# Kernel optimization log

Hardware: AMD Instinct MI355X
Metric: run time of the kernel (lower is better)

Reference implementation:

```python
import math
import jax, jax.numpy as jnp
import numpy as np

DIM = 1024
HEADS = 16
HEAD_DIM = DIM // HEADS
NEG = -10000.0


def setup_inputs() -> dict:
    key = jax.random.key(0)
    ks = jax.random.split(key, 9)
    B, S = 2, 2048
    s = 1.0 / math.sqrt(DIM)
    inp = {
        "x": jax.random.normal(ks[0], (B, S, DIM), dtype=jnp.float32),
        "Wq": jax.random.normal(ks[1], (DIM, DIM), dtype=jnp.float32) * s,
        "bq": jnp.zeros((DIM,), dtype=jnp.float32),
        "Wk": jax.random.normal(ks[2], (DIM, DIM), dtype=jnp.float32) * s,
        "bk": jnp.zeros((DIM,), dtype=jnp.float32),
        "Wv": jax.random.normal(ks[3], (DIM, DIM), dtype=jnp.float32) * s,
        "bv": jnp.zeros((DIM,), dtype=jnp.float32),
        "Wo": jax.random.normal(ks[4], (DIM, DIM), dtype=jnp.float32) * s,
        "bo": jnp.zeros((DIM,), dtype=jnp.float32),
    }
    return inp


def reference(x, Wq, bq, Wk, bk, Wv, bv, Wo, bo):
    B, S, D = x.shape
    q = x @ Wq + bq
    k = x @ Wk + bk
    v = x @ Wv + bv
    # [B, H, S, hd]
    def split_heads(t):
        return t.reshape(B, S, HEADS, HEAD_DIM).transpose(0, 2, 1, 3)
    q, k, v = split_heads(q), split_heads(k), split_heads(v)
    scores = jnp.einsum("bhqd,bhkd->bhqk", q, k) / math.sqrt(HEAD_DIM)
    causal = jnp.tril(jnp.ones((S, S), dtype=bool))  # [S, S]
    scores = jnp.where(causal[None, None], scores, NEG)
    probs = jax.nn.softmax(scores, axis=-1)
    ctx = jnp.einsum("bhqk,bhkd->bhqd", probs, v)  # [B, H, S, hd]
    ctx = ctx.transpose(0, 2, 1, 3).reshape(B, S, D)
    out = ctx @ Wo + bo
    return out
```

## Files before the change

### kernel.cpp

```cpp
#include <hip/hip_runtime.h>
#include <hip/hip_bf16.h>
#include <math.h>

#define DIMX 1024
#define HEADSX 16
#define HDX 64
#define BBX 2
#define SSX 2048
#define MMX (BBX*SSX)

typedef __bf16 bf16x8 __attribute__((ext_vector_type(8)));
typedef __bf16 bf16x4 __attribute__((ext_vector_type(4)));
typedef float  f32x4  __attribute__((ext_vector_type(4)));

#define NEGF (-1e30f)
#define QSCALE 0.18033688011112042f

static __device__ __forceinline__ void gload16(const void* g, void* l) {
  __builtin_amdgcn_global_load_lds(
      (const __attribute__((address_space(1))) unsigned int*)g,
      (__attribute__((address_space(3))) unsigned int*)l, 16, 0, 0);
}

__global__ __launch_bounds__(256) void k_convert_x(const float* __restrict__ x,
                                                   __bf16* __restrict__ xb) {
  int i = (blockIdx.x * 256 + threadIdx.x) * 4;
  float4 v = *(const float4*)&x[i];
  bf16x4 o = { (__bf16)v.x, (__bf16)v.y, (__bf16)v.z, (__bf16)v.w };
  *(bf16x4*)&xb[i] = o;
}

__global__ __launch_bounds__(256) void k_transpose_w(
    const float* __restrict__ Wq, const float* __restrict__ Wk,
    const float* __restrict__ Wv, const float* __restrict__ Wo,
    __bf16* __restrict__ wqkvT, __bf16* __restrict__ woT) {
  __shared__ __bf16 tile[64][65];
  const int mat = blockIdx.y;
  const float* src = (mat == 0) ? Wq : (mat == 1) ? Wk : (mat == 2) ? Wv : Wo;
  __bf16* dst = (mat < 3) ? (wqkvT + (size_t)mat * DIMX * DIMX) : woT;
  const int tx = blockIdx.x & 15, ty = blockIdx.x >> 4;
  const int k0 = ty * 64, n0 = tx * 64;
  #pragma unroll
  for (int rep = 0; rep < 16; ++rep) {
    int idx = rep * 256 + threadIdx.x;
    int r = idx >> 6, c = idx & 63;
    tile[r][c] = (__bf16)src[(size_t)(k0 + r) * DIMX + n0 + c];
  }
  __syncthreads();
  #pragma unroll
  for (int rep = 0; rep < 16; ++rep) {
    int idx = rep * 256 + threadIdx.x;
    int r = idx >> 6, c = idx & 63;
    dst[(size_t)(n0 + r) * DIMX + k0 + c] = tile[c][r];
  }
}

__global__ __launch_bounds__(256) void k_gemm_qkv(
    const __bf16* __restrict__ A,
    const __bf16* __restrict__ Bt,
    const float* __restrict__ b0, const float* __restrict__ b1,
    const float* __restrict__ b2,
    __bf16* __restrict__ qb, __bf16* __restrict__ kb, __bf16* __restrict__ vtb) {
  constexpr int BK = 32, K = 1024;
  __shared__ __bf16 As[128 * BK];
  __shared__ __bf16 Bs[128 * BK];
  const int tid = threadIdx.x, lane = tid & 63, wave = tid >> 6;
  const int g = lane >> 4, r16 = lane & 15;
  const int wm = wave & 1, wn = wave >> 1;
  const int id = blockIdx.x;
  const int xcd = id & 7, j96 = id >> 3;
  const int m0 = (xcd * 4 + (j96 & 3)) * 128;
  const int n0 = (j96 >> 2) * 128;

  f32x4 acc[4][4] = {};

  for (int k0 = 0; k0 < K; k0 += BK) {
    __syncthreads();
    #pragma unroll
    for (int i = 0; i < 2; ++i) {
      int c = wave * 64 + lane + 256 * i;
      gload16(&A [(size_t)(m0 + (c >> 2)) * K + k0 + (c & 3) * 8],
              (char*)As + (size_t)(wave * 64 + 256 * i) * 16);
      gload16(&Bt[(size_t)(n0 + (c >> 2)) * K + k0 + (c & 3) * 8],
              (char*)Bs + (size_t)(wave * 64 + 256 * i) * 16);
    }
    __syncthreads();
    bf16x8 af[4], bfr[4];
    #pragma unroll
    for (int i = 0; i < 4; ++i)
      af[i]  = *(const bf16x8*)&As[(wm * 64 + i * 16 + r16) * BK + g * 8];
    #pragma unroll
    for (int j = 0; j < 4; ++j)
      bfr[j] = *(const bf16x8*)&Bs[(wn * 64 + j * 16 + r16) * BK + g * 8];
    #pragma unroll
    for (int i = 0; i < 4; ++i)
      #pragma unroll
      for (int j = 0; j < 4; ++j)
        acc[i][j] = __builtin_amdgcn_mfma_f32_16x16x32_bf16(af[i], bfr[j],
                                                            acc[i][j], 0, 0, 0);
  }

  #pragma unroll
  for (int i = 0; i < 4; ++i) {
    #pragma unroll
    for (int j = 0; j < 4; ++j) {
      #pragma unroll
      for (int r = 0; r < 4; ++r) {
        int m = m0 + wm * 64 + i * 16 + 4 * g + r;
        int n = n0 + wn * 64 + j * 16 + r16;
        float v = acc[i][j][r];
        int proj = n >> 10, w = n & 1023, h = w >> 6, d = w & 63;
        const float* bp = (proj == 0) ? b0 : (proj == 1) ? b1 : b2;
        v += bp[w];
        int b = m >> 11, s = m & 2047, bh = b * HEADSX + h;
        if (proj == 0)      qb [((size_t)bh * SSX + s) * HDX + d] =
                                (__bf16)(v * QSCALE);
        else if (proj == 1) kb [((size_t)bh * SSX + s) * HDX + d] = (__bf16)v;
        else                vtb[((size_t)bh * HDX + d) * SSX + s] = (__bf16)v;
      }
    }
  }
}

__global__ __launch_bounds__(256) void k_gemm_out(
    const __bf16* __restrict__ A,
    const __bf16* __restrict__ Bt,
    const float* __restrict__ bias, float* __restrict__ outf) {
  constexpr int BK = 32, K = 1024;
  __shared__ __bf16 As[64 * BK];
  __shared__ __bf16 Bs[64 * BK];
  const int tid = threadIdx.x, lane = tid & 63, wave = tid >> 6;
  const int g = lane >> 4, r16 = lane & 15;
  const int wm = wave & 1, wn = wave >> 1;
  const int id = blockIdx.x;
  const int xcd = id & 7, j128 = id >> 3;
  const int m0 = (xcd * 8 + (j128 & 7)) * 64;
  const int n0 = (j128 >> 3) * 64;

  f32x4 acc[2][2] = {};

  for (int k0 = 0; k0 < K; k0 += BK) {
    __syncthreads();
    {
      int c = tid;
      gload16(&A [(size_t)(m0 + (c >> 2)) * K + k0 + (c & 3) * 8],
              (char*)As + (size_t)(wave * 64) * 16);
      gload16(&Bt[(size_t)(n0 + (c >> 2)) * K + k0 + (c & 3) * 8],
              (char*)Bs + (size_t)(wave * 64) * 16);
    }
    __syncthreads();
    bf16x8 af[2], bfr[2];
    #pragma unroll
    for (int i = 0; i < 2; ++i)
      af[i]  = *(const bf16x8*)&As[(wm * 32 + i * 16 + r16) * BK + g * 8];
    #pragma unroll
    for (int j = 0; j < 2; ++j)
      bfr[j] = *(const bf16x8*)&Bs[(wn * 32 + j * 16 + r16) * BK + g * 8];
    #pragma unroll
    for (int i = 0; i < 2; ++i)
      #pragma unroll
      for (int j = 0; j < 2; ++j)
        acc[i][j] = __builtin_amdgcn_mfma_f32_16x16x32_bf16(af[i], bfr[j],
                                                            acc[i][j], 0, 0, 0);
  }

  #pragma unroll
  for (int i = 0; i < 2; ++i)
    #pragma unroll
    for (int j = 0; j < 2; ++j)
      #pragma unroll
      for (int r = 0; r < 4; ++r) {
        int m = m0 + wm * 32 + i * 16 + 4 * g + r;
        int n = n0 + wn * 32 + j * 16 + r16;
        outf[(size_t)m * DIMX + n] = acc[i][j][r] + bias[n];
      }
}

__global__ __launch_bounds__(256, 2) void k_attn(
    const __bf16* __restrict__ qb, const __bf16* __restrict__ kb,
    const __bf16* __restrict__ vtb, __bf16* __restrict__ ctxb) {
  const int tid = threadIdx.x;
  const int lane = tid & 63, wq = tid >> 6;
  const int g = lane >> 4, r16 = lane & 15;

  const int id = blockIdx.x;
  const int xcd = id & 7, idx = id >> 3;
  const int bh = xcd * 4 + (idx & 3);
  const int p  = idx >> 2;
  const int b = bh >> 4, h = bh & 15;

  const int ntL = p + 1, ntH = 32 - p;
  const int q0L = p * 64 + wq * 16;
  const int q0H = (31 - p) * 64 + wq * 16;

  const __bf16* Q  = qb  + (size_t)bh * SSX * HDX;
  const __bf16* Kp = kb  + (size_t)bh * SSX * HDX;
  const __bf16* Vt = vtb + (size_t)bh * HDX * SSX;

  __shared__ __bf16 Ks[2][64 * 64];
  __shared__ __bf16 Vs[2][64 * 64];
  __shared__ unsigned Pld[4][512];

  bf16x8 qfL[2], qfH[2];
  qfL[0] = *(const bf16x8*)&Q[(size_t)(q0L + r16) * HDX + g * 8];
  qfL[1] = *(const bf16x8*)&Q[(size_t)(q0L + r16) * HDX + 32 + g * 8];
  qfH[0] = *(const bf16x8*)&Q[(size_t)(q0H + r16) * HDX + g * 8];
  qfH[1] = *(const bf16x8*)&Q[(size_t)(q0H + r16) * HDX + 32 + g * 8];

  f32x4 accL[4] = {}, accH[4] = {};
  float mrunL = NEGF, lrunL = 0.f;
  float mrunH = NEGF, lrunH = 0.f;

  auto STAGE = [&](int buf, int t) {
    const int kv0 = t * 64;
    #pragma unroll
    for (int i = 0; i < 2; ++i) {
      int c = tid + 256 * i;
      int r = c >> 3;
      int cb = (c & 7) ^ (r & 7);
      gload16(&Kp[(size_t)(kv0 + r) * HDX + cb * 8],
              (char*)Ks[buf] + (size_t)(wq * 64 + 256 * i) * 16);
      gload16(&Vt[(size_t)r * SSX + kv0 + cb * 8],
              (char*)Vs[buf] + (size_t)(wq * 64 + 256 * i) * 16);
    }
  };

  auto SUBTILE = [&](const bf16x8* qf, f32x4* acc, float& mrun, float& lrun,
                     int qrow, bool last, int kv0, int cur) {
    f32x4 sac[4] = {};
    __builtin_amdgcn_s_setprio(1);
    #pragma unroll
    for (int kk = 0; kk < 2; ++kk)
      #pragma unroll
      for (int jj = 0; jj < 4; ++jj) {
        int rr = jj * 16 + r16;
        bf16x8 kf = *(const bf16x8*)
            &Ks[cur][rr * 64 + (((kk << 2) + g) ^ (rr & 7)) * 8];
        sac[jj] = __builtin_amdgcn_mfma_f32_16x16x32_bf16(kf, qf[kk], sac[jj],
                                                          0, 0, 0);
      }
    __builtin_amdgcn_s_setprio(0);

    float pv[4][4];
    float mt = NEGF;
    #pragma unroll
    for (int jj = 0; jj < 4; ++jj)
      #pragma unroll
      for (int r = 0; r < 4; ++r) {
        float s = sac[jj][r];
        if (last) {
          int kcol = kv0 + jj * 16 + 4 * g + r;
          s = (kcol > qrow) ? NEGF : s;
        }
        pv[jj][r] = s;
        mt = fmaxf(mt, s);
      }
    mt = fmaxf(mt, __shfl_xor(mt, 16));
    mt = fmaxf(mt, __shfl_xor(mt, 32));

    if (__any(mt > mrun)) {
      float mnew = fmaxf(mrun, mt);
      float fac = exp2f(mrun - mnew);
      mrun = mnew;
      lrun *= fac;
      #pragma unroll
      for (int j2 = 0; j2 < 4; ++j2)
        #pragma unroll
        for (int r = 0; r < 4; ++r)
          acc[j2][r] *= fac;
    }

    float rs = 0.f;
    #pragma unroll
    for (int jj = 0; jj < 4; ++jj)
      #pragma unroll
      for (int r = 0; r < 4; ++r) {
        float px = exp2f(pv[jj][r] - mrun);
        pv[jj][r] = px;
        rs += px;
      }
    lrun += rs;

    #pragma unroll
    for (int jj = 0; jj < 4; ++jj)
      #pragma unroll
      for (int rp = 0; rp < 2; ++rp) {
        unsigned w;
        asm("v_cvt_pk_bf16_f32 %0, %1, %2"
            : "=v"(w) : "v"(pv[jj][2 * rp]), "v"(pv[jj][2 * rp + 1]));
        int c = jj * 8 + g * 2 + rp;
        int addr = r16 * 32 + (((c >> 2) ^ (r16 & 7)) << 2) + (c & 3);
        Pld[wq][addr] = w;
      }

    bf16x8 pf[2];
    #pragma unroll
    for (int half = 0; half < 2; ++half) {
      int c = half * 16 + g * 4;
      int addr = r16 * 32 + (((c >> 2) ^ (r16 & 7)) << 2);
      pf[half] = *(const bf16x8*)&Pld[wq][addr];
    }
    __builtin_amdgcn_s_setprio(1);
    #pragma unroll
    for (int j2 = 0; j2 < 4; ++j2)
      #pragma unroll
      for (int half = 0; half < 2; ++half) {
        int dd = j2 * 16 + r16;
        bf16x8 vf = *(const bf16x8*)
            &Vs[cur][dd * 64 + (((half << 2) + g) ^ (dd & 7)) * 8];
        acc[j2] = __builtin_amdgcn_mfma_f32_16x16x32_bf16(vf, pf[half],
                                                          acc[j2], 0, 0, 0);
      }
    __builtin_amdgcn_s_setprio(0);
  };

  STAGE(0, 0);
  __syncthreads();

  for (int t = 0; t < ntH; ++t) {
    const int cur = t & 1;
    if (t + 1 < ntH) STAGE(cur ^ 1, t + 1);
    const int kv0 = t * 64;

    SUBTILE(qfH, accH, mrunH, lrunH, q0H + r16, t == ntH - 1, kv0, cur);
    if (t < ntL)
      SUBTILE(qfL, accL, mrunL, lrunL, q0L + r16, t == ntL - 1, kv0, cur);

    __syncthreads();
  }

  auto EPIL = [&](f32x4* acc, float lrun, int q0) {
    lrun += __shfl_xor(lrun, 16);
    lrun += __shfl_xor(lrun, 32);
    const float inv = 1.f / lrun;
    const int s = q0 + r16;
    #pragma unroll
    for (int j2 = 0; j2 < 4; ++j2)
      #pragma unroll
      for (int r = 0; r < 4; ++r) {
        int d = j2 * 16 + 4 * g + r;
        ctxb[((size_t)(b * SSX + s)) * DIMX + h * HDX + d] =
            (__bf16)(acc[j2][r] * inv);
      }
  };
  EPIL(accH, lrunH, q0H);
  EPIL(accL, lrunL, q0L);
}

extern "C" void kernel_launch(void* const* d_in, const int* in_sizes, int n_in,
                              void* d_out, int out_size, void* d_ws,
                              size_t ws_size, hipStream_t stream) {
  const float* x  = (const float*)d_in[0];
  const float* Wq = (const float*)d_in[1];
  const float* bq = (const float*)d_in[2];
  const float* Wk = (const float*)d_in[3];
  const float* bk = (const float*)d_in[4];
  const float* Wv = (const float*)d_in[5];
  const float* bv = (const float*)d_in[6];
  const float* Wo = (const float*)d_in[7];
  const float* bo = (const float*)d_in[8];
  float* out = (float*)d_out;

  char* ws = (char*)d_ws;
  __bf16* xb    = (__bf16*)(ws);
  __bf16* wqkvT = (__bf16*)(ws + ((size_t)8  << 20));
  __bf16* woT   = (__bf16*)(ws + ((size_t)14 << 20));
  __bf16* qb    = (__bf16*)(ws + ((size_t)16 << 20));
  __bf16* kb    = (__bf16*)(ws + ((size_t)24 << 20));
  __bf16* vtb   = (__bf16*)(ws + ((size_t)32 << 20));
  __bf16* ctxb  = xb;

  k_convert_x<<<4096, 256, 0, stream>>>(x, xb);
  k_transpose_w<<<dim3(256, 4), 256, 0, stream>>>(Wq, Wk, Wv, Wo, wqkvT, woT);
  k_gemm_qkv<<<768, 256, 0, stream>>>(xb, wqkvT, bq, bk, bv, qb, kb, vtb);
  k_attn<<<512, 256, 0, stream>>>(qb, kb, vtb, ctxb);
  k_gemm_out<<<1024, 256, 0, stream>>>(ctxb, woT, bo, out);
}
```

Before: 118.5 us.

## Interleave attention subtiles, enlarge output GEMM tile, fuse prep kernels

The attention loop now computes both the high and low query subtiles' QK MFMAs together in one pass. This shares each K fragment load and gives the scheduler independent MFMA chains to overlap. The loop is split into a phase with both subtiles and a high-only phase, and each wave gets a separate P buffer per subtile. The output GEMM moves from 64x64 to 128x64 tiles with half the blocks, which raises data reuse per block. The x conversion and weight transpose are merged into one launch to cut launch overhead. Costs are more registers and shared memory per block, which could lower occupancy.

```diff
diff --git a/kernel.cpp b/kernel.cpp
--- a/kernel.cpp
+++ b/kernel.cpp
@@ -16,29 +16,33 @@
 #define NEGF (-1e30f)
 #define QSCALE 0.18033688011112042f
 
+template<bool B> struct BoolC { static constexpr bool value = B; };
+
 static __device__ __forceinline__ void gload16(const void* g, void* l) {
   __builtin_amdgcn_global_load_lds(
       (const __attribute__((address_space(1))) unsigned int*)g,
       (__attribute__((address_space(3))) unsigned int*)l, 16, 0, 0);
 }
 
-__global__ __launch_bounds__(256) void k_convert_x(const float* __restrict__ x,
-                                                   __bf16* __restrict__ xb) {
-  int i = (blockIdx.x * 256 + threadIdx.x) * 4;
-  float4 v = *(const float4*)&x[i];
-  bf16x4 o = { (__bf16)v.x, (__bf16)v.y, (__bf16)v.z, (__bf16)v.w };
-  *(bf16x4*)&xb[i] = o;
-}
-
-__global__ __launch_bounds__(256) void k_transpose_w(
-    const float* __restrict__ Wq, const float* __restrict__ Wk,
-    const float* __restrict__ Wv, const float* __restrict__ Wo,
+__global__ __launch_bounds__(256) void k_prep(
+    const float* __restrict__ x, const float* __restrict__ Wq,
+    const float* __restrict__ Wk, const float* __restrict__ Wv,
+    const float* __restrict__ Wo, __bf16* __restrict__ xb,
     __bf16* __restrict__ wqkvT, __bf16* __restrict__ woT) {
+  const int bid = blockIdx.x;
+  if (bid < 4096) {
+    int i = (bid * 256 + threadIdx.x) * 4;
+    float4 v = *(const float4*)&x[i];
+    bf16x4 o = { (__bf16)v.x, (__bf16)v.y, (__bf16)v.z, (__bf16)v.w };
+    *(bf16x4*)&xb[i] = o;
+    return;
+  }
   __shared__ __bf16 tile[64][65];
-  const int mat = blockIdx.y;
+  const int wb = bid - 4096;
+  const int mat = wb >> 8, t8 = wb & 255;
   const float* src = (mat == 0) ? Wq : (mat == 1) ? Wk : (mat == 2) ? Wv : Wo;
   __bf16* dst = (mat < 3) ? (wqkvT + (size_t)mat * DIMX * DIMX) : woT;
-  const int tx = blockIdx.x & 15, ty = blockIdx.x >> 4;
+  const int tx = t8 & 15, ty = t8 >> 4;
   const int k0 = ty * 64, n0 = tx * 64;
   #pragma unroll
   for (int rep = 0; rep < 16; ++rep) {
@@ -127,37 +131,41 @@
     const __bf16* __restrict__ Bt,
     const float* __restrict__ bias, float* __restrict__ outf) {
   constexpr int BK = 32, K = 1024;
-  __shared__ __bf16 As[64 * BK];
+  __shared__ __bf16 As[128 * BK];
   __shared__ __bf16 Bs[64 * BK];
   const int tid = threadIdx.x, lane = tid & 63, wave = tid >> 6;
   const int g = lane >> 4, r16 = lane & 15;
   const int wm = wave & 1, wn = wave >> 1;
   const int id = blockIdx.x;
-  const int xcd = id & 7, j128 = id >> 3;
-  const int m0 = (xcd * 8 + (j128 & 7)) * 64;
-  const int n0 = (j128 >> 3) * 64;
-
-  f32x4 acc[2][2] = {};
+  const int xcd = id & 7, j64 = id >> 3;
+  const int m0 = (xcd * 4 + (j64 & 3)) * 128;
+  const int n0 = (j64 >> 2) * 64;
+
+  f32x4 acc[4][2] = {};
 
   for (int k0 = 0; k0 < K; k0 += BK) {
     __syncthreads();
+    #pragma unroll
+    for (int i = 0; i < 2; ++i) {
+      int c = wave * 64 + lane + 256 * i;
+      gload16(&A [(size_t)(m0 + (c >> 2)) * K + k0 + (c & 3) * 8],
+              (char*)As + (size_t)(wave * 64 + 256 * i) * 16);
+    }
     {
       int c = tid;
-      gload16(&A [(size_t)(m0 + (c >> 2)) * K + k0 + (c & 3) * 8],
-              (char*)As + (size_t)(wave * 64) * 16);
       gload16(&Bt[(size_t)(n0 + (c >> 2)) * K + k0 + (c & 3) * 8],
               (char*)Bs + (size_t)(wave * 64) * 16);
     }
     __syncthreads();
-    bf16x8 af[2], bfr[2];
-    #pragma unroll
-    for (int i = 0; i < 2; ++i)
-      af[i]  = *(const bf16x8*)&As[(wm * 32 + i * 16 + r16) * BK + g * 8];
+    bf16x8 af[4], bfr[2];
+    #pragma unroll
+    for (int i = 0; i < 4; ++i)
+      af[i]  = *(const bf16x8*)&As[(wm * 64 + i * 16 + r16) * BK + g * 8];
     #pragma unroll
     for (int j = 0; j < 2; ++j)
       bfr[j] = *(const bf16x8*)&Bs[(wn * 32 + j * 16 + r16) * BK + g * 8];
     #pragma unroll
-    for (int i = 0; i < 2; ++i)
+    for (int i = 0; i < 4; ++i)
       #pragma unroll
       for (int j = 0; j < 2; ++j)
         acc[i][j] = __builtin_amdgcn_mfma_f32_16x16x32_bf16(af[i], bfr[j],
@@ -165,12 +173,12 @@
   }
 
   #pragma unroll
-  for (int i = 0; i < 2; ++i)
+  for (int i = 0; i < 4; ++i)
     #pragma unroll
     for (int j = 0; j < 2; ++j)
       #pragma unroll
       for (int r = 0; r < 4; ++r) {
-        int m = m0 + wm * 32 + i * 16 + 4 * g + r;
+        int m = m0 + wm * 64 + i * 16 + 4 * g + r;
         int n = n0 + wn * 32 + j * 16 + r16;
         outf[(size_t)m * DIMX + n] = acc[i][j][r] + bias[n];
       }
@@ -199,7 +207,7 @@
 
   __shared__ __bf16 Ks[2][64 * 64];
   __shared__ __bf16 Vs[2][64 * 64];
-  __shared__ unsigned Pld[4][512];
+  __shared__ unsigned Pld[8][512];
 
   bf16x8 qfL[2], qfH[2];
   qfL[0] = *(const bf16x8*)&Q[(size_t)(q0L + r16) * HDX + g * 8];
@@ -225,22 +233,8 @@
     }
   };
 
-  auto SUBTILE = [&](const bf16x8* qf, f32x4* acc, float& mrun, float& lrun,
-                     int qrow, bool last, int kv0, int cur) {
-    f32x4 sac[4] = {};
-    __builtin_amdgcn_s_setprio(1);
-    #pragma unroll
-    for (int kk = 0; kk < 2; ++kk)
-      #pragma unroll
-      for (int jj = 0; jj < 4; ++jj) {
-        int rr = jj * 16 + r16;
-        bf16x8 kf = *(const bf16x8*)
-            &Ks[cur][rr * 64 + (((kk << 2) + g) ^ (rr & 7)) * 8];
-        sac[jj] = __builtin_amdgcn_mfma_f32_16x16x32_bf16(kf, qf[kk], sac[jj],
-                                                          0, 0, 0);
-      }
-    __builtin_amdgcn_s_setprio(0);
-
+  auto SM = [&](f32x4* sac, f32x4* acc, float& mrun, float& lrun,
+                int qrow, bool last, int kv0, unsigned* pld) {
     float pv[4][4];
     float mt = NEGF;
     #pragma unroll
@@ -257,7 +251,6 @@
       }
     mt = fmaxf(mt, __shfl_xor(mt, 16));
     mt = fmaxf(mt, __shfl_xor(mt, 32));
-
     if (__any(mt > mrun)) {
       float mnew = fmaxf(mrun, mt);
       float fac = exp2f(mrun - mnew);
@@ -269,7 +262,6 @@
         for (int r = 0; r < 4; ++r)
           acc[j2][r] *= fac;
     }
-
     float rs = 0.f;
     #pragma unroll
     for (int jj = 0; jj < 4; ++jj)
@@ -280,7 +272,6 @@
         rs += px;
       }
     lrun += rs;
-
     #pragma unroll
     for (int jj = 0; jj < 4; ++jj)
       #pragma unroll
@@ -290,15 +281,45 @@
             : "=v"(w) : "v"(pv[jj][2 * rp]), "v"(pv[jj][2 * rp + 1]));
         int c = jj * 8 + g * 2 + rp;
         int addr = r16 * 32 + (((c >> 2) ^ (r16 & 7)) << 2) + (c & 3);
-        Pld[wq][addr] = w;
-      }
-
-    bf16x8 pf[2];
+        pld[addr] = w;
+      }
+  };
+
+  auto STEP = [&](auto dolc, int t, bool lastH) {
+    constexpr bool doL = decltype(dolc)::value;
+    const int cur = t & 1;
+    if (t + 1 < ntH) STAGE(cur ^ 1, t + 1);
+    const int kv0 = t * 64;
+
+    f32x4 sacH[4] = {}, sacL[4] = {};
+    __builtin_amdgcn_s_setprio(1);
+    #pragma unroll
+    for (int kk = 0; kk < 2; ++kk)
+      #pragma unroll
+      for (int jj = 0; jj < 4; ++jj) {
+        int rr = jj * 16 + r16;
+        bf16x8 kf = *(const bf16x8*)
+            &Ks[cur][rr * 64 + (((kk << 2) + g) ^ (rr & 7)) * 8];
+        sacH[jj] = __builtin_amdgcn_mfma_f32_16x16x32_bf16(kf, qfH[kk],
+                                                           sacH[jj], 0, 0, 0);
+        if constexpr (doL)
+          sacL[jj] = __builtin_amdgcn_mfma_f32_16x16x32_bf16(kf, qfL[kk],
+                                                             sacL[jj], 0, 0, 0);
+      }
+    __builtin_amdgcn_s_setprio(0);
+
+    SM(sacH, accH, mrunH, lrunH, q0H + r16, lastH, kv0, &Pld[wq * 2][0]);
+    if constexpr (doL)
+      SM(sacL, accL, mrunL, lrunL, q0L + r16, t == ntL - 1, kv0,
+         &Pld[wq * 2 + 1][0]);
+
+    bf16x8 pfH[2], pfL[2];
     #pragma unroll
     for (int half = 0; half < 2; ++half) {
       int c = half * 16 + g * 4;
       int addr = r16 * 32 + (((c >> 2) ^ (r16 & 7)) << 2);
-      pf[half] = *(const bf16x8*)&Pld[wq][addr];
+      pfH[half] = *(const bf16x8*)&Pld[wq * 2][addr];
+      if constexpr (doL) pfL[half] = *(const bf16x8*)&Pld[wq * 2 + 1][addr];
     }
     __builtin_amdgcn_s_setprio(1);
     #pragma unroll
@@ -308,8 +329,11 @@
         int dd = j2 * 16 + r16;
         bf16x8 vf = *(const bf16x8*)
             &Vs[cur][dd * 64 + (((half << 2) + g) ^ (dd & 7)) * 8];
-        acc[j2] = __builtin_amdgcn_mfma_f32_16x16x32_bf16(vf, pf[half],
-                                                          acc[j2], 0, 0, 0);
+        accH[j2] = __builtin_amdgcn_mfma_f32_16x16x32_bf16(vf, pfH[half],
+                                                           accH[j2], 0, 0, 0);
+        if constexpr (doL)
+          accL[j2] = __builtin_amdgcn_mfma_f32_16x16x32_bf16(vf, pfL[half],
+                                                             accL[j2], 0, 0, 0);
       }
     __builtin_amdgcn_s_setprio(0);
   };
@@ -317,15 +341,13 @@
   STAGE(0, 0);
   __syncthreads();
 
-  for (int t = 0; t < ntH; ++t) {
-    const int cur = t & 1;
-    if (t + 1 < ntH) STAGE(cur ^ 1, t + 1);
-    const int kv0 = t * 64;
-
-    SUBTILE(qfH, accH, mrunH, lrunH, q0H + r16, t == ntH - 1, kv0, cur);
-    if (t < ntL)
-      SUBTILE(qfL, accL, mrunL, lrunL, q0L + r16, t == ntL - 1, kv0, cur);
-
+  int t = 0;
+  for (; t < ntL; ++t) {
+    STEP(BoolC<true>{}, t, false);
+    __syncthreads();
+  }
+  for (; t < ntH; ++t) {
+    STEP(BoolC<false>{}, t, t == ntH - 1);
     __syncthreads();
   }
 
@@ -370,9 +392,8 @@
   __bf16* vtb   = (__bf16*)(ws + ((size_t)32 << 20));
   __bf16* ctxb  = xb;
 
-  k_convert_x<<<4096, 256, 0, stream>>>(x, xb);
-  k_transpose_w<<<dim3(256, 4), 256, 0, stream>>>(Wq, Wk, Wv, Wo, wqkvT, woT);
+  k_prep<<<5120, 256, 0, stream>>>(x, Wq, Wk, Wv, Wo, xb, wqkvT, woT);
   k_gemm_qkv<<<768, 256, 0, stream>>>(xb, wqkvT, bq, bk, bv, qb, kb, vtb);
   k_attn<<<512, 256, 0, stream>>>(qb, kb, vtb, ctxb);
-  k_gemm_out<<<1024, 256, 0, stream>>>(ctxb, woT, bo, out);
-}
+  k_gemm_out<<<512, 256, 0, stream>>>(ctxb, woT, bo, out);
+}
```

Result: no change. 117.5 us (-0.8%).
